# Optimization experiments

Hardware: AMD Instinct MI355X
Metric: run time of the kernel (lower is better)

## Reference

```python
import jax, jax.numpy as jnp
import numpy as np

# ---- Cl(3,0) Cayley table; blade order [1, e1,e2,e3, e12,e13,e23, e123] ----
def _build_cayley():
    blades = [0b000, 0b001, 0b010, 0b100, 0b011, 0b101, 0b110, 0b111]
    pos = {b: i for i, b in enumerate(blades)}
    def sign(a, b):
        s, a = 0, a >> 1
        while a:
            s += bin(a & b).count('1')
            a >>= 1
        return -1.0 if s & 1 else 1.0
    C = np.zeros((8, 8, 8), np.float32)
    for i, a in enumerate(blades):
        for k, b in enumerate(blades):
            C[i, pos[a ^ b], k] = sign(a, b)  # e_a * e_b -> sign * e_(a^b), metric all +1
    return jnp.asarray(C)

CAYLEY = _build_cayley()
EPS = 1e-6
SEQ = 25      # num_nodes (5) + num_edges (20)
HEADS = 8

def _expand_grades(w):
    # [..., 4] (per-grade) -> [..., 8] (per-blade), grade dims 1,3,3,1
    return jnp.concatenate([w[..., 0:1],
                            jnp.repeat(w[..., 1:2], 3, -1),
                            jnp.repeat(w[..., 2:3], 3, -1),
                            w[..., 3:4]], axis=-1)

def mv_linear(x, w, b):
    # x [N, in, 8], w [out, in, 4], b [out]; bias only on scalar blade
    y = jnp.einsum('nmi,omi->noi', x, _expand_grades(w))
    return y.at[..., 0].add(b)

def mv_layernorm(x, a):
    n = jnp.linalg.norm(x, axis=-1, keepdims=True)   # [N, c, 1] multivector norm
    n = jnp.mean(n, axis=1, keepdims=True) + EPS     # mean over channels -> [N, 1, 1]
    return a[None, :, None] * x / n

def mv_silu(x, a, b):
    # invariants: scalar component + squared grade magnitudes (mag2)
    inv = jnp.stack([x[..., 0],
                     jnp.sum(x[..., 1:4] ** 2, -1),
                     jnp.sum(x[..., 4:7] ** 2, -1),
                     x[..., 7] ** 2], axis=-1)       # [N, c, 4]
    return _expand_grades(jax.nn.sigmoid(a * inv + b)) * x

def geometric_product(a, b):
    return jnp.einsum('nci,ijk,nck->ncj', a, CAYLEY, b)


def setup_inputs() -> dict:
    key = jax.random.key(0)
    ks = iter(jax.random.split(key, 40))
    D, B = 128, 1024
    N = B * SEQ
    s = 0.05
    rn = lambda *sh: jax.random.normal(next(ks), sh, jnp.float32) * s
    return dict(
        src=jax.random.normal(next(ks), (N, D, 8), jnp.float32),
        ln1_a=jnp.ones(D, jnp.float32), ln2_a=jnp.ones(D, jnp.float32), ln3_a=jnp.ones(D, jnp.float32),
        wq=rn(D, D, 4), bq=jnp.zeros(D, jnp.float32),
        wk=rn(D, D, 4), bk=jnp.zeros(D, jnp.float32),
        wv=rn(D, D, 4), bv=jnp.zeros(D, jnp.float32),
        wo=rn(D, D, 4), bo=jnp.zeros(D, jnp.float32),
        gw1=rn(2 * D, D, 4), gb1=jnp.zeros(2 * D, jnp.float32),
        gw2=rn(2 * D, D, 4), gb2=jnp.zeros(2 * D, jnp.float32),
        gw3=rn(D, 2 * D, 4), gb3=jnp.zeros(D, jnp.float32),
        gna=jnp.ones(D, jnp.float32),
        mw1=rn(2 * D, D, 4), mb1=jnp.zeros(2 * D, jnp.float32),
        sa=jnp.ones((2 * D, 4), jnp.float32), sb=jnp.zeros((2 * D, 4), jnp.float32),
        mw2=rn(D, 2 * D, 4), mb2=jnp.zeros(D, jnp.float32),
    )


def reference(src, ln1_a, ln2_a, ln3_a, wq, bq, wk, bk, wv, bv, wo, bo,
              gw1, gb1, gw2, gb2, gw3, gb3, gna,
              mw1, mb1, sa, sb, mw2, mb2):
    N, D, _ = src.shape
    B, dh = N // SEQ, D // HEADS

    def attention(x):
        q = mv_linear(x, wq, bq).reshape(B, SEQ, HEADS, dh, 8)
        k = mv_linear(x, wk, bk).reshape(B, SEQ, HEADS, dh, 8)
        v = mv_linear(x, wv, bv).reshape(B, SEQ, HEADS, dh, 8)
        scores = jnp.einsum('bshdi,bthdi->bhst', q, k) / np.float32(np.sqrt(dh * 8))
        p = jax.nn.softmax(scores, axis=-1)
        o = jnp.einsum('bhst,bthdi->bshdi', p, v).reshape(N, D, 8)
        return mv_linear(o, wo, bo)

    # pre-norm attention + residual
    x = src + attention(mv_layernorm(src, ln1_a))
    x = mv_layernorm(x, ln2_a)
    # GP_Layer: two grade-wise linears -> geometric product -> linear -> norm
    xl = mv_linear(x, gw1, gb1)
    xr = mv_linear(x, gw2, gb2)
    g = mv_layernorm(mv_linear(geometric_product(xl, xr), gw3, gb3), gna)
    x = x + g
    x = mv_layernorm(x, ln3_a)
    # gated MLP: MVLinear -> MVSiLU -> MVLinear
    ff = mv_linear(mv_silu(mv_linear(x, mw1, mb1), sa, sb), mw2, mb2)
    return x + ff
```

## Files before the change

kernel.cpp:

```cpp
#include <hip/hip_runtime.h>
#include <hip/hip_bf16.h>
#include <math.h>

#define NROWS 25600
#define SEQL  25
#define EPSV  1e-6f

typedef __hip_bfloat16 bf16;
typedef __attribute__((ext_vector_type(4))) float f32x4;
typedef __attribute__((ext_vector_type(8))) short bf16x8;
typedef __attribute__((ext_vector_type(4))) short s16x4;
typedef unsigned int u32;

#define GLD16(gp_, lp_) __builtin_amdgcn_global_load_lds( \
    (const __attribute__((address_space(1))) u32*)(gp_), \
    (__attribute__((address_space(3))) u32*)(lp_), 16, 0, 0)

__device__ __forceinline__ float b2f(short s) {
  return __uint_as_float(((u32)(unsigned short)s) << 16);
}
__device__ __forceinline__ short f2b(float f) {
  __hip_bfloat16 h = __float2bfloat16(f);
  return *reinterpret_cast<short*>(&h);
}

__device__ __forceinline__ void gprod(const float* a, const float* b, float* r) {
  const int M[8] = {0,1,2,4,3,5,6,7};
  const int P[8] = {0,1,2,4,3,5,6,7};
#pragma unroll
  for (int i = 0; i < 8; ++i) {
    const int ma = M[i];
#pragma unroll
    for (int k = 0; k < 8; ++k) {
      const int mb = M[k];
      int par = 0;
      for (int t = ma >> 1; t; t >>= 1) par += __popc(t & mb);
      const float s = (par & 1) ? -1.f : 1.f;
      r[P[ma ^ mb]] += s * a[i] * b[k];
    }
  }
}

struct G8 {
  const bf16* A; const bf16* W; const float* bias; const float* invnm;
  bf16* Y0; bf16* Y1; bf16* Y2; bf16* Y3;
  int yc0, yc1, yc2, yc3; int ONW; int ONS;
};

#define OPITCH 84

template<int KT>
__global__ __launch_bounds__(256, 5) void gemm10_kernel(G8 P)
{
  __shared__ __align__(16) short As[64 * 128];
  __shared__ __align__(16) short Bs[64 * 128];
  const int tid  = threadIdx.x;
  const int lane = tid & 63;
  const int wid  = tid >> 6;
  const int z    = blockIdx.z;
  const int g    = (z == 0) ? 0 : ((z < 4) ? 1 : ((z < 7) ? 2 : 3));
  const int by   = blockIdx.y;
  const size_t n0 = (size_t)blockIdx.x * 64;
  const bf16* Ab = P.A + (size_t)z * NROWS * KT + n0 * KT;
  const bf16* Wb = P.W + ((size_t)g * P.ONW + by * 64) * KT;
  const int bufi = by >> 1;
  bf16* Yb; int yc;
  if      (bufi == 0) { Yb = P.Y0; yc = P.yc0; }
  else if (bufi == 1) { Yb = P.Y1; yc = P.yc1; }
  else if (bufi == 2) { Yb = P.Y2; yc = P.yc2; }
  else                { Yb = P.Y3; yc = P.yc3; }
  yc += (by & 1) * 64;

  f32x4 acc[2][2];
#pragma unroll
  for (int i = 0; i < 2; ++i)
#pragma unroll
    for (int j = 0; j < 2; ++j) acc[i][j] = (f32x4){0.f, 0.f, 0.f, 0.f};

  const int wm = (wid & 1) * 32;
  const int wn = (wid >> 1) * 32;
  const int lg  = lane >> 4;
  const int c8  = lane & 15;
  const int l15 = lane & 15;

  constexpr int NC = KT / 128;
#pragma unroll
  for (int kc = 0; kc < NC; ++kc) {
#pragma unroll
    for (int j = 0; j < 4; ++j) {
      const int row = wid * 16 + j * 4 + lg;
      const int sw = (c8 ^ (row & 7)) * 8;
      GLD16(Ab + (size_t)row * KT + kc * 128 + sw, &As[wid * 2048 + j * 512]);
      GLD16(Wb + (size_t)row * KT + kc * 128 + sw, &Bs[wid * 2048 + j * 512]);
    }
    __syncthreads();
#pragma unroll
    for (int ks = 0; ks < 4; ++ks) {
      bf16x8 af[2], bg[2];
#pragma unroll
      for (int i = 0; i < 2; ++i) {
        const int rA = wm + i * 16 + l15;
        const int rB = wn + i * 16 + l15;
        af[i] = *(const bf16x8*)&As[rA * 128 + (((ks * 4 + lg) ^ (rA & 7)) * 8)];
        bg[i] = *(const bf16x8*)&Bs[rB * 128 + (((ks * 4 + lg) ^ (rB & 7)) * 8)];
      }
#pragma unroll
      for (int mi = 0; mi < 2; ++mi)
#pragma unroll
        for (int ni = 0; ni < 2; ++ni)
          acc[mi][ni] = __builtin_amdgcn_mfma_f32_16x16x32_bf16(af[mi], bg[ni], acc[mi][ni], 0, 0, 0);
    }
    __syncthreads();
  }

  short* Os = As;
  const int cr = lg * 4;
#pragma unroll
  for (int mi = 0; mi < 2; ++mi) {
#pragma unroll
    for (int j = 0; j < 4; ++j) {
      const int r = wm + mi * 16 + cr + j;
      const size_t n = n0 + r;
      const float sc = P.invnm ? P.invnm[n] : 1.f;
#pragma unroll
      for (int ni = 0; ni < 2; ++ni) {
        const int cl = wn + ni * 16 + l15;
        float v = acc[mi][ni][j] * sc;
        if (z == 0) v += P.bias[by * 64 + cl];
        Os[r * OPITCH + cl] = f2b(v);
      }
    }
  }
  __syncthreads();

  bf16* Yp = Yb + (size_t)z * NROWS * P.ONS + yc;
  const int wrow = tid >> 3;
  const int wcol = (tid & 7) * 8;
#pragma unroll
  for (int rr = 0; rr < 2; ++rr) {
    const int row = rr * 32 + wrow;
    const s16x4 lo = *(const s16x4*)&Os[row * OPITCH + wcol];
    const s16x4 hi = *(const s16x4*)&Os[row * OPITCH + wcol + 4];
    *(s16x4*)(Yp + (size_t)(n0 + row) * P.ONS + wcol) = lo;
    *(s16x4*)(Yp + (size_t)(n0 + row) * P.ONS + wcol + 4) = hi;
  }
}

__global__ __launch_bounds__(256) void wprep_all_kernel(
    const float* wq, const float* wk, const float* wv, const float* wo,
    const float* gw1, const float* gw2, const float* gw3,
    const float* mw1, const float* mw2,
    const float* ln1, const float* ln2, const float* ln3,
    bf16* WQKV, bf16* WO, bf16* WG12, bf16* WG3, bf16* WM1, bf16* WM2)
{
  const int gid = blockIdx.x * 256 + threadIdx.x;
  const float* w; const float* ln; bf16* out; int K; int idx; int planeSz; int rowOfs;
  if      (gid <  16384) { w=wq;  ln=ln1;     out=WQKV; K=128; idx=gid;        planeSz=49152; rowOfs=0;   }
  else if (gid <  32768) { w=wk;  ln=ln1;     out=WQKV; K=128; idx=gid-16384;  planeSz=49152; rowOfs=128; }
  else if (gid <  49152) { w=wv;  ln=ln1;     out=WQKV; K=128; idx=gid-32768;  planeSz=49152; rowOfs=256; }
  else if (gid <  65536) { w=wo;  ln=nullptr; out=WO;   K=128; idx=gid-49152;  planeSz=16384; rowOfs=0;   }
  else if (gid <  98304) { w=gw1; ln=ln2;     out=WG12; K=128; idx=gid-65536;  planeSz=65536; rowOfs=0;   }
  else if (gid < 131072) { w=gw2; ln=ln2;     out=WG12; K=128; idx=gid-98304;  planeSz=65536; rowOfs=256; }
  else if (gid < 163840) { w=gw3; ln=nullptr; out=WG3;  K=256; idx=gid-131072; planeSz=32768; rowOfs=0;   }
  else if (gid < 196608) { w=mw1; ln=ln3;     out=WM1;  K=128; idx=gid-163840; planeSz=32768; rowOfs=0;   }
  else                   { w=mw2; ln=nullptr; out=WM2;  K=256; idx=gid-196608; planeSz=32768; rowOfs=0;   }
  const int k = idx % K;
  const float s = ln ? ln[k] : 1.f;
  const float4 wv4 = *(const float4*)(w + (size_t)idx * 4);
  bf16* dst = out + (size_t)rowOfs * K + idx;
  dst[0 * planeSz] = __float2bfloat16(wv4.x * s);
  dst[1 * planeSz] = __float2bfloat16(wv4.y * s);
  dst[2 * planeSz] = __float2bfloat16(wv4.z * s);
  dst[3 * planeSz] = __float2bfloat16(wv4.w * s);
}

__global__ __launch_bounds__(256) void bias_prep_kernel(
    const float* bq, const float* bk, const float* bv,
    const float* gb1, const float* gb2,
    float* BQKV, float* BG12)
{
  const int t = blockIdx.x * 256 + threadIdx.x;
  if      (t < 128) BQKV[t] = bq[t];
  else if (t < 256) BQKV[t] = bk[t - 128];
  else if (t < 384) BQKV[t] = bv[t - 256];
  else if (t < 640) BG12[t - 384] = gb1[t - 384];
  else if (t < 896) BG12[t - 384] = gb2[t - 640];
}

__global__ __launch_bounds__(256) void repack_kernel(
    const float* __restrict__ src, bf16* __restrict__ Xp, float* __restrict__ nminv)
{
  const int tid = threadIdx.x;
  const size_t base = ((size_t)blockIdx.x * 256 + tid) * 4;
  const size_t P = (size_t)NROWS * 128;
  float v[4][8];
  const float4* sp = (const float4*)(src + base * 8);
  float part = 0.f;
#pragma unroll
  for (int e = 0; e < 4; ++e) {
    const float4 a = sp[e * 2], b = sp[e * 2 + 1];
    v[e][0]=a.x; v[e][1]=a.y; v[e][2]=a.z; v[e][3]=a.w;
    v[e][4]=b.x; v[e][5]=b.y; v[e][6]=b.z; v[e][7]=b.w;
    float ss = 0.f;
#pragma unroll
    for (int p = 0; p < 8; ++p) ss += v[e][p] * v[e][p];
    part += sqrtf(ss);
  }
#pragma unroll
  for (int p = 0; p < 8; ++p) {
    s16x4 o;
#pragma unroll
    for (int e = 0; e < 4; ++e) o[e] = f2b(v[e][p]);
    *(s16x4*)(Xp + p * P + base) = o;
  }
#pragma unroll
  for (int off = 1; off < 32; off <<= 1) part += __shfl_xor(part, off);
  if ((tid & 31) == 0) nminv[base >> 7] = 1.f / (part / 128.f + EPSV);
}

__global__ __launch_bounds__(256) void attn_kernel(
    bf16* __restrict__ Q, const bf16* __restrict__ K, const bf16* __restrict__ V)
{
  __shared__ float Pld[4][32 * 36];
  const int tid  = threadIdx.x;
  const int lane = tid & 63;
  const int wid  = tid >> 6;
  const int job  = blockIdx.x * 4 + wid;
  const int b    = job >> 3;
  const int h    = job & 7;
  const size_t PS = (size_t)NROWS * 128;
  const int rowbase = b * SEQL;
  const int l15 = lane & 15;
  const int lg  = lane >> 4;

  f32x4 acc[2][2];
#pragma unroll
  for (int si = 0; si < 2; ++si)
#pragma unroll
    for (int ti = 0; ti < 2; ++ti) acc[si][ti] = (f32x4){0.f,0.f,0.f,0.f};

#pragma unroll
  for (int ks = 0; ks < 4; ++ks) {
    const int f = ks * 32 + lg * 8;
    const int p = f >> 4, d = f & 15;
    bf16x8 aq[2], bk[2];
#pragma unroll
    for (int si = 0; si < 2; ++si) {
      int s = si * 16 + l15; if (s > 24) s = 24;
      aq[si] = *(const bf16x8*)(Q + (size_t)p * PS + (size_t)(rowbase + s) * 128 + h * 16 + d);
    }
#pragma unroll
    for (int ti = 0; ti < 2; ++ti) {
      int t = ti * 16 + l15; if (t > 24) t = 24;
      bk[ti] = *(const bf16x8*)(K + (size_t)p * PS + (size_t)(rowbase + t) * 128 + h * 16 + d);
    }
#pragma unroll
    for (int si = 0; si < 2; ++si)
#pragma unroll
      for (int ti = 0; ti < 2; ++ti)
        acc[si][ti] = __builtin_amdgcn_mfma_f32_16x16x32_bf16(aq[si], bk[ti], acc[si][ti], 0, 0, 0);
  }

  const float scale = 0.08838834764831845f;
  float pv[2][2][4];
#pragma unroll
  for (int si = 0; si < 2; ++si)
#pragma unroll
    for (int ti = 0; ti < 2; ++ti)
#pragma unroll
      for (int r = 0; r < 4; ++r) {
        float v = acc[si][ti][r] * scale;
        if (ti * 16 + l15 > 24) v = -1e30f;
        pv[si][ti][r] = v;
      }
#pragma unroll
  for (int si = 0; si < 2; ++si)
#pragma unroll
    for (int r = 0; r < 4; ++r) {
      float m = fmaxf(pv[si][0][r], pv[si][1][r]);
#pragma unroll
      for (int off = 1; off < 16; off <<= 1) m = fmaxf(m, __shfl_xor(m, off));
      const float e0 = __expf(pv[si][0][r] - m);
      const float e1 = __expf(pv[si][1][r] - m);
      float sum = e0 + e1;
#pragma unroll
      for (int off = 1; off < 16; off <<= 1) sum += __shfl_xor(sum, off);
      const float inv = 1.f / sum;
      pv[si][0][r] = e0 * inv;
      pv[si][1][r] = e1 * inv;
    }

  float* Pw = &Pld[wid][0];
#pragma unroll
  for (int si = 0; si < 2; ++si)
#pragma unroll
    for (int ti = 0; ti < 2; ++ti)
#pragma unroll
      for (int r = 0; r < 4; ++r)
        Pw[(si * 16 + lg * 4 + r) * 36 + ti * 16 + l15] = pv[si][ti][r];
  __syncthreads();

  const int p2 = lane >> 3;
  const int d2 = (lane & 7) * 2;
  const bf16* vb = V + (size_t)p2 * PS + (size_t)rowbase * 128 + h * 16 + d2;
  float vlo[32], vhi[32];
#pragma unroll
  for (int t = 0; t < SEQL; ++t) {
    const __hip_bfloat162 vv = *(const __hip_bfloat162*)(vb + (size_t)t * 128);
    vlo[t] = __bfloat162float(vv.x);
    vhi[t] = __bfloat162float(vv.y);
  }
#pragma unroll
  for (int t = SEQL; t < 32; ++t) { vlo[t] = 0.f; vhi[t] = 0.f; }

  bf16* ob = Q + (size_t)p2 * PS + (size_t)rowbase * 128 + h * 16 + d2;
  for (int s = 0; s < SEQL; ++s) {
    const float4* pr = reinterpret_cast<const float4*>(&Pld[wid][s * 36]);
    float a0 = 0.f, a1 = 0.f;
#pragma unroll
    for (int t4 = 0; t4 < 8; ++t4) {
      const float4 pq = pr[t4];
      a0 += pq.x * vlo[t4*4+0] + pq.y * vlo[t4*4+1] + pq.z * vlo[t4*4+2] + pq.w * vlo[t4*4+3];
      a1 += pq.x * vhi[t4*4+0] + pq.y * vhi[t4*4+1] + pq.z * vhi[t4*4+2] + pq.w * vhi[t4*4+3];
    }
    __hip_bfloat162 o2;
    o2.x = __float2bfloat16(a0);
    o2.y = __float2bfloat16(a1);
    *(__hip_bfloat162*)(ob + (size_t)s * 128) = o2;
  }
}

__global__ __launch_bounds__(256) void xres_kernel(
    const float* __restrict__ src, const bf16* __restrict__ AO,
    bf16* __restrict__ X, float* __restrict__ nminv)
{
  const int tid = threadIdx.x;
  const size_t base = ((size_t)blockIdx.x * 256 + tid) * 4;
  const size_t P = (size_t)NROWS * 128;
  float v[4][8];
  const float4* sp = (const float4*)(src + base * 8);
#pragma unroll
  for (int e = 0; e < 4; ++e) {
    const float4 a = sp[e * 2], b = sp[e * 2 + 1];
    v[e][0]=a.x; v[e][1]=a.y; v[e][2]=a.z; v[e][3]=a.w;
    v[e][4]=b.x; v[e][5]=b.y; v[e][6]=b.z; v[e][7]=b.w;
  }
  float part = 0.f;
  float ss[4] = {0.f, 0.f, 0.f, 0.f};
#pragma unroll
  for (int p = 0; p < 8; ++p) {
    const s16x4 av = *(const s16x4*)(AO + p * P + base);
    s16x4 o;
#pragma unroll
    for (int e = 0; e < 4; ++e) {
      v[e][p] += b2f(av[e]);
      o[e] = f2b(v[e][p]);
      ss[e] += v[e][p] * v[e][p];
    }
    *(s16x4*)(X + p * P + base) = o;
  }
#pragma unroll
  for (int e = 0; e < 4; ++e) part += sqrtf(ss[e]);
#pragma unroll
  for (int off = 1; off < 32; off <<= 1) part += __shfl_xor(part, off);
  if ((tid & 31) == 0) nminv[base >> 7] = 1.f / (part / 128.f + EPSV);
}

__global__ __launch_bounds__(256) void gp_kernel(
    bf16* __restrict__ XL, const bf16* __restrict__ XR)
{
  const size_t base = ((size_t)blockIdx.x * 256 + threadIdx.x) * 4;
  const size_t P = (size_t)NROWS * 256;
  s16x4 av[8], bv[8], rv[8];
#pragma unroll
  for (int p = 0; p < 8; ++p) {
    av[p] = *(const s16x4*)(XL + p * P + base);
    bv[p] = *(const s16x4*)(XR + p * P + base);
  }
#pragma unroll
  for (int e = 0; e < 4; ++e) {
    float a[8], b[8], r[8] = {0.f,0.f,0.f,0.f,0.f,0.f,0.f,0.f};
#pragma unroll
    for (int p = 0; p < 8; ++p) { a[p] = b2f(av[p][e]); b[p] = b2f(bv[p][e]); }
    gprod(a, b, r);
#pragma unroll
    for (int p = 0; p < 8; ++p) rv[p][e] = f2b(r[p]);
  }
#pragma unroll
  for (int p = 0; p < 8; ++p) *(s16x4*)(XL + p * P + base) = rv[p];
}

__global__ __launch_bounds__(256) void combine_kernel(
    bf16* __restrict__ X, const bf16* __restrict__ Gl,
    const float* __restrict__ ln2a, const float* __restrict__ gna,
    const float* __restrict__ nm2inv, float* __restrict__ nm4inv)
{
  const int tid = threadIdx.x;
  const size_t base = ((size_t)blockIdx.x * 256 + tid) * 4;
  const size_t P = (size_t)NROWS * 128;
  const size_t n = base >> 7;
  const int c = (int)(base & 127);

  float gv[4][8];
  float ssg[4] = {0.f,0.f,0.f,0.f};
#pragma unroll
  for (int p = 0; p < 8; ++p) {
    const s16x4 g4 = *(const s16x4*)(Gl + p * P + base);
#pragma unroll
    for (int e = 0; e < 4; ++e) { gv[e][p] = b2f(g4[e]); ssg[e] += gv[e][p] * gv[e][p]; }
  }
  float partg = sqrtf(ssg[0]) + sqrtf(ssg[1]) + sqrtf(ssg[2]) + sqrtf(ssg[3]);
#pragma unroll
  for (int off = 1; off < 32; off <<= 1) partg += __shfl_xor(partg, off);
  const float invg = 1.f / (partg / 128.f + EPSV);

  const float n2 = nm2inv[n];
  float s2[4], sg[4];
#pragma unroll
  for (int e = 0; e < 4; ++e) { s2[e] = ln2a[c + e] * n2; sg[e] = gna[c + e] * invg; }

  float ss[4] = {0.f,0.f,0.f,0.f};
#pragma unroll
  for (int p = 0; p < 8; ++p) {
    const s16x4 x4 = *(const s16x4*)(X + p * P + base);
    s16x4 o;
#pragma unroll
    for (int e = 0; e < 4; ++e) {
      const float v = s2[e] * b2f(x4[e]) + sg[e] * gv[e][p];
      o[e] = f2b(v);
      ss[e] += v * v;
    }
    *(s16x4*)(X + p * P + base) = o;
  }
  float part = sqrtf(ss[0]) + sqrtf(ss[1]) + sqrtf(ss[2]) + sqrtf(ss[3]);
#pragma unroll
  for (int off = 1; off < 32; off <<= 1) part += __shfl_xor(part, off);
  if ((tid & 31) == 0) nm4inv[n] = 1.f / (part / 128.f + EPSV);
}

__global__ __launch_bounds__(256) void silu_kernel(
    bf16* __restrict__ H, const float* __restrict__ sa, const float* __restrict__ sb)
{
  const size_t base = ((size_t)blockIdx.x * 256 + threadIdx.x) * 4;
  const int c = (int)(base & 255);
  const size_t P = (size_t)NROWS * 256;
  s16x4 hv[8];
#pragma unroll
  for (int p = 0; p < 8; ++p) hv[p] = *(const s16x4*)(H + p * P + base);
#pragma unroll
  for (int e = 0; e < 4; ++e) {
    float v[8];
#pragma unroll
    for (int p = 0; p < 8; ++p) v[p] = b2f(hv[p][e]);
    const float i0 = v[0];
    const float i1 = v[1]*v[1] + v[2]*v[2] + v[3]*v[3];
    const float i2 = v[4]*v[4] + v[5]*v[5] + v[6]*v[6];
    const float i3 = v[7]*v[7];
    const int cc = c + e;
    const float g0 = 1.f / (1.f + __expf(-(sa[cc*4+0]*i0 + sb[cc*4+0])));
    const float g1 = 1.f / (1.f + __expf(-(sa[cc*4+1]*i1 + sb[cc*4+1])));
    const float g2 = 1.f / (1.f + __expf(-(sa[cc*4+2]*i2 + sb[cc*4+2])));
    const float g3 = 1.f / (1.f + __expf(-(sa[cc*4+3]*i3 + sb[cc*4+3])));
    v[0]*=g0; v[1]*=g1; v[2]*=g1; v[3]*=g1; v[4]*=g2; v[5]*=g2; v[6]*=g2; v[7]*=g3;
#pragma unroll
    for (int p = 0; p < 8; ++p) hv[p][e] = f2b(v[p]);
  }
#pragma unroll
  for (int p = 0; p < 8; ++p) *(s16x4*)(H + p * P + base) = hv[p];
}

__global__ __launch_bounds__(256) void final_kernel(
    const bf16* __restrict__ X3, const bf16* __restrict__ FF,
    const float* __restrict__ ln3a, const float* __restrict__ nm4inv,
    float* __restrict__ out)
{
  const size_t base = ((size_t)blockIdx.x * 256 + threadIdx.x) * 4;
  const int c = (int)(base & 127);
  const size_t n = base >> 7;
  const size_t P = (size_t)NROWS * 128;
  const float nm = nm4inv[n];
  float o[4][8];
#pragma unroll
  for (int p = 0; p < 8; ++p) {
    const s16x4 x4 = *(const s16x4*)(X3 + p * P + base);
    const s16x4 f4 = *(const s16x4*)(FF + p * P + base);
#pragma unroll
    for (int e = 0; e < 4; ++e)
      o[e][p] = ln3a[c + e] * nm * b2f(x4[e]) + b2f(f4[e]);
  }
  float4* op = (float4*)(out + base * 8);
#pragma unroll
  for (int e = 0; e < 4; ++e) {
    float4 lo, hi;
    lo.x=o[e][0]; lo.y=o[e][1]; lo.z=o[e][2]; lo.w=o[e][3];
    hi.x=o[e][4]; hi.y=o[e][5]; hi.z=o[e][6]; hi.w=o[e][7];
    op[e * 2] = lo;
    op[e * 2 + 1] = hi;
  }
}

extern "C" void kernel_launch(void* const* d_in, const int* in_sizes, int n_in,
                              void* d_out, int out_size, void* d_ws, size_t ws_size,
                              hipStream_t stream) {
  (void)in_sizes; (void)n_in; (void)out_size; (void)ws_size;
  const float* src   = (const float*)d_in[0];
  const float* ln1_a = (const float*)d_in[1];
  const float* ln2_a = (const float*)d_in[2];
  const float* ln3_a = (const float*)d_in[3];
  const float* wq = (const float*)d_in[4];  const float* bq = (const float*)d_in[5];
  const float* wk = (const float*)d_in[6];  const float* bk = (const float*)d_in[7];
  const float* wv = (const float*)d_in[8];  const float* bv = (const float*)d_in[9];
  const float* wo = (const float*)d_in[10]; const float* bo = (const float*)d_in[11];
  const float* gw1 = (const float*)d_in[12]; const float* gb1 = (const float*)d_in[13];
  const float* gw2 = (const float*)d_in[14]; const float* gb2 = (const float*)d_in[15];
  const float* gw3 = (const float*)d_in[16]; const float* gb3 = (const float*)d_in[17];
  const float* gna = (const float*)d_in[18];
  const float* mw1 = (const float*)d_in[19]; const float* mb1 = (const float*)d_in[20];
  const float* sa  = (const float*)d_in[21]; const float* sb  = (const float*)d_in[22];
  const float* mw2 = (const float*)d_in[23]; const float* mb2 = (const float*)d_in[24];

  char* ws = (char*)d_ws;
  const size_t P128 = (size_t)NROWS * 128;
  const size_t PSET = 8 * P128;
  bf16* R1 = (bf16*)ws;
  bf16* R2 = (bf16*)(ws + 104857600);
  bf16* WQKV = (bf16*)(ws + 157286400);
  bf16* WO   = WQKV + 196608;
  bf16* WG12 = WO   + 65536;
  bf16* WG3  = WG12 + 262144;
  bf16* WM1  = WG3  + 131072;
  bf16* WM2  = WM1  + 131072;
  float* BQKV = (float*)(ws + 159121408);
  float* BG12 = BQKV + 384;
  float* nm1  = BG12 + 512;
  float* nm2  = nm1 + NROWS;
  float* nm4  = nm2 + NROWS;

  bf16* Dd = (bf16*)d_out;
  bf16* Kb = R1;
  bf16* Vb = R1 + PSET;

  wprep_all_kernel<<<896, 256, 0, stream>>>(
      wq, wk, wv, wo, gw1, gw2, gw3, mw1, mw2, ln1_a, ln2_a, ln3_a,
      WQKV, WO, WG12, WG3, WM1, WM2);
  bias_prep_kernel<<<4, 256, 0, stream>>>(bq, bk, bv, gb1, gb2, BQKV, BG12);

  repack_kernel<<<3200, 256, 0, stream>>>(src, R2, nm1);

  G8 P{};
  P = G8{R2, WQKV, BQKV, nm1, Dd, Kb, Vb, nullptr, 0,0,0,0, 384, 128};
  gemm10_kernel<128><<<dim3(400, 6, 8), 256, 0, stream>>>(P);

  attn_kernel<<<2048, 256, 0, stream>>>(Dd, Kb, Vb);

  P = G8{Dd, WO, bo, nullptr, R1, nullptr, nullptr, nullptr, 0,0,0,0, 128, 128};
  gemm10_kernel<128><<<dim3(400, 2, 8), 256, 0, stream>>>(P);

  xres_kernel<<<3200, 256, 0, stream>>>(src, R1, R2, nm2);

  P = G8{R2, WG12, BG12, nm2, Dd, Dd, R1, R1, 0, 128, 0, 128, 512, 256};
  gemm10_kernel<128><<<dim3(400, 8, 8), 256, 0, stream>>>(P);

  gp_kernel<<<6400, 256, 0, stream>>>(Dd, R1);

  P = G8{Dd, WG3, gb3, nullptr, R1, nullptr, nullptr, nullptr, 0,0,0,0, 128, 128};
  gemm10_kernel<256><<<dim3(400, 2, 8), 256, 0, stream>>>(P);

  combine_kernel<<<3200, 256, 0, stream>>>(R2, R1, ln2_a, gna, nm2, nm4);

  P = G8{R2, WM1, mb1, nm4, Dd, Dd, nullptr, nullptr, 0, 128, 0, 0, 256, 256};
  gemm10_kernel<128><<<dim3(400, 4, 8), 256, 0, stream>>>(P);

  silu_kernel<<<6400, 256, 0, stream>>>(Dd, sa, sb);

  P = G8{Dd, WM2, mb2, nullptr, R1, nullptr, nullptr, nullptr, 0,0,0,0, 128, 128};
  gemm10_kernel<256><<<dim3(400, 2, 8), 256, 0, stream>>>(P);

  final_kernel<<<3200, 256, 0, stream>>>(R2, R1, ln3_a, nm4, (float*)d_out);
}
```

Before: 583.0 us.

## Keep A tile resident in LDS and loop over output column tiles in-block

The GEMM kernel now stages the 64-row activation tile once into shared memory and loops over all output column tiles inside the block, restaging only the weight tile per column tile. Previously each column tile was a separate block that reloaded the same activation rows. This cuts the number of blocks and the redundant global reads of activations. In exchange, shared memory per block grows (up to 64 KB+ for KT=256), occupancy drops (launch bounds hint removed), and the weight restage is not overlapped with compute.

```diff
diff --git a/kernel.cpp b/kernel.cpp
--- a/kernel.cpp
+++ b/kernel.cpp
@@ -41,7 +41,7 @@
   }
 }
 
-struct G8 {
+struct G11 {
   const bf16* A; const bf16* W; const float* bias; const float* invnm;
   bf16* Y0; bf16* Y1; bf16* Y2; bf16* Y3;
   int yc0, yc1, yc2, yc3; int ONW; int ONS;
@@ -49,100 +49,115 @@
 
 #define OPITCH 84
 
-template<int KT>
-__global__ __launch_bounds__(256, 5) void gemm10_kernel(G8 P)
-{
-  __shared__ __align__(16) short As[64 * 128];
-  __shared__ __align__(16) short Bs[64 * 128];
+template<int KT, int NCOL>
+__global__ __launch_bounds__(256) void gemm11_kernel(G11 P)
+{
+  constexpr int NC = KT / 128;
+  __shared__ __align__(16) short As[64 * KT];
+  __shared__ __align__(16) short Ws[64 * KT];
+  __shared__ __align__(16) short Cs[64 * OPITCH];
   const int tid  = threadIdx.x;
   const int lane = tid & 63;
   const int wid  = tid >> 6;
   const int z    = blockIdx.z;
   const int g    = (z == 0) ? 0 : ((z < 4) ? 1 : ((z < 7) ? 2 : 3));
-  const int by   = blockIdx.y;
   const size_t n0 = (size_t)blockIdx.x * 64;
   const bf16* Ab = P.A + (size_t)z * NROWS * KT + n0 * KT;
-  const bf16* Wb = P.W + ((size_t)g * P.ONW + by * 64) * KT;
-  const int bufi = by >> 1;
-  bf16* Yb; int yc;
-  if      (bufi == 0) { Yb = P.Y0; yc = P.yc0; }
-  else if (bufi == 1) { Yb = P.Y1; yc = P.yc1; }
-  else if (bufi == 2) { Yb = P.Y2; yc = P.yc2; }
-  else                { Yb = P.Y3; yc = P.yc3; }
-  yc += (by & 1) * 64;
-
-  f32x4 acc[2][2];
-#pragma unroll
-  for (int i = 0; i < 2; ++i)
-#pragma unroll
-    for (int j = 0; j < 2; ++j) acc[i][j] = (f32x4){0.f, 0.f, 0.f, 0.f};
-
-  const int wm = (wid & 1) * 32;
-  const int wn = (wid >> 1) * 32;
+  const int wm  = (wid & 1) * 32;
+  const int wn  = (wid >> 1) * 32;
   const int lg  = lane >> 4;
-  const int c8  = lane & 15;
   const int l15 = lane & 15;
 
-  constexpr int NC = KT / 128;
-#pragma unroll
-  for (int kc = 0; kc < NC; ++kc) {
+  auto STAGEW = [&](int ct) {
+    const bf16* Wb = P.W + ((size_t)g * P.ONW + ct * 64) * KT;
+#pragma unroll
+    for (int kc = 0; kc < NC; ++kc)
+#pragma unroll
+      for (int j = 0; j < 4; ++j) {
+        const int row = wid * 16 + j * 4 + lg;
+        const int sw = (l15 ^ (row & 7)) * 8;
+        GLD16(Wb + (size_t)row * KT + kc * 128 + sw, &Ws[kc * 8192 + wid * 2048 + j * 512]);
+      }
+  };
+
+#pragma unroll
+  for (int kc = 0; kc < NC; ++kc)
 #pragma unroll
     for (int j = 0; j < 4; ++j) {
       const int row = wid * 16 + j * 4 + lg;
-      const int sw = (c8 ^ (row & 7)) * 8;
-      GLD16(Ab + (size_t)row * KT + kc * 128 + sw, &As[wid * 2048 + j * 512]);
-      GLD16(Wb + (size_t)row * KT + kc * 128 + sw, &Bs[wid * 2048 + j * 512]);
+      const int sw = (l15 ^ (row & 7)) * 8;
+      GLD16(Ab + (size_t)row * KT + kc * 128 + sw, &As[kc * 8192 + wid * 2048 + j * 512]);
+    }
+  STAGEW(0);
+  __syncthreads();
+
+#pragma unroll
+  for (int ct = 0; ct < NCOL; ++ct) {
+    f32x4 acc[2][2];
+#pragma unroll
+    for (int i = 0; i < 2; ++i)
+#pragma unroll
+      for (int j = 0; j < 2; ++j) acc[i][j] = (f32x4){0.f, 0.f, 0.f, 0.f};
+#pragma unroll
+    for (int kc = 0; kc < NC; ++kc) {
+#pragma unroll
+      for (int ks = 0; ks < 4; ++ks) {
+        bf16x8 af[2], bg[2];
+#pragma unroll
+        for (int i = 0; i < 2; ++i) {
+          const int rA = wm + i * 16 + l15;
+          const int rB = wn + i * 16 + l15;
+          af[i] = *(const bf16x8*)&As[kc * 8192 + rA * 128 + (((ks * 4 + lg) ^ (rA & 7)) * 8)];
+          bg[i] = *(const bf16x8*)&Ws[kc * 8192 + rB * 128 + (((ks * 4 + lg) ^ (rB & 7)) * 8)];
+        }
+#pragma unroll
+        for (int mi = 0; mi < 2; ++mi)
+#pragma unroll
+          for (int ni = 0; ni < 2; ++ni)
+            acc[mi][ni] = __builtin_amdgcn_mfma_f32_16x16x32_bf16(af[mi], bg[ni], acc[mi][ni], 0, 0, 0);
+      }
+    }
+
+    const int cr = lg * 4;
+#pragma unroll
+    for (int mi = 0; mi < 2; ++mi) {
+#pragma unroll
+      for (int j = 0; j < 4; ++j) {
+        const int r = wm + mi * 16 + cr + j;
+        const size_t n = n0 + r;
+        const float sc = P.invnm ? P.invnm[n] : 1.f;
+#pragma unroll
+        for (int ni = 0; ni < 2; ++ni) {
+          const int cl = wn + ni * 16 + l15;
+          float v = acc[mi][ni][j] * sc;
+          if (z == 0) v += P.bias[ct * 64 + cl];
+          Cs[r * OPITCH + cl] = f2b(v);
+        }
+      }
     }
     __syncthreads();
-#pragma unroll
-    for (int ks = 0; ks < 4; ++ks) {
-      bf16x8 af[2], bg[2];
-#pragma unroll
-      for (int i = 0; i < 2; ++i) {
-        const int rA = wm + i * 16 + l15;
-        const int rB = wn + i * 16 + l15;
-        af[i] = *(const bf16x8*)&As[rA * 128 + (((ks * 4 + lg) ^ (rA & 7)) * 8)];
-        bg[i] = *(const bf16x8*)&Bs[rB * 128 + (((ks * 4 + lg) ^ (rB & 7)) * 8)];
-      }
-#pragma unroll
-      for (int mi = 0; mi < 2; ++mi)
-#pragma unroll
-        for (int ni = 0; ni < 2; ++ni)
-          acc[mi][ni] = __builtin_amdgcn_mfma_f32_16x16x32_bf16(af[mi], bg[ni], acc[mi][ni], 0, 0, 0);
+
+    if (ct + 1 < NCOL) STAGEW(ct + 1);
+
+    const int bufi = ct >> 1;
+    bf16* Yb; int yc;
+    if      (bufi == 0) { Yb = P.Y0; yc = P.yc0; }
+    else if (bufi == 1) { Yb = P.Y1; yc = P.yc1; }
+    else if (bufi == 2) { Yb = P.Y2; yc = P.yc2; }
+    else                { Yb = P.Y3; yc = P.yc3; }
+    yc += (ct & 1) * 64;
+    bf16* Yp = Yb + (size_t)z * NROWS * P.ONS + yc;
+    const int wrow = tid >> 3;
+    const int wcol = (tid & 7) * 8;
+#pragma unroll
+    for (int rr = 0; rr < 2; ++rr) {
+      const int row = rr * 32 + wrow;
+      const s16x4 lo = *(const s16x4*)&Cs[row * OPITCH + wcol];
+      const s16x4 hi = *(const s16x4*)&Cs[row * OPITCH + wcol + 4];
+      *(s16x4*)(Yp + (size_t)(n0 + row) * P.ONS + wcol) = lo;
+      *(s16x4*)(Yp + (size_t)(n0 + row) * P.ONS + wcol + 4) = hi;
     }
     __syncthreads();
-  }
-
-  short* Os = As;
-  const int cr = lg * 4;
-#pragma unroll
-  for (int mi = 0; mi < 2; ++mi) {
-#pragma unroll
-    for (int j = 0; j < 4; ++j) {
-      const int r = wm + mi * 16 + cr + j;
-      const size_t n = n0 + r;
-      const float sc = P.invnm ? P.invnm[n] : 1.f;
-#pragma unroll
-      for (int ni = 0; ni < 2; ++ni) {
-        const int cl = wn + ni * 16 + l15;
-        float v = acc[mi][ni][j] * sc;
-        if (z == 0) v += P.bias[by * 64 + cl];
-        Os[r * OPITCH + cl] = f2b(v);
-      }
-    }
-  }
-  __syncthreads();
-
-  bf16* Yp = Yb + (size_t)z * NROWS * P.ONS + yc;
-  const int wrow = tid >> 3;
-  const int wcol = (tid & 7) * 8;
-#pragma unroll
-  for (int rr = 0; rr < 2; ++rr) {
-    const int row = rr * 32 + wrow;
-    const s16x4 lo = *(const s16x4*)&Os[row * OPITCH + wcol];
-    const s16x4 hi = *(const s16x4*)&Os[row * OPITCH + wcol + 4];
-    *(s16x4*)(Yp + (size_t)(n0 + row) * P.ONS + wcol) = lo;
-    *(s16x4*)(Yp + (size_t)(n0 + row) * P.ONS + wcol + 4) = hi;
   }
 }
 
@@ -547,34 +562,34 @@
 
   repack_kernel<<<3200, 256, 0, stream>>>(src, R2, nm1);
 
-  G8 P{};
-  P = G8{R2, WQKV, BQKV, nm1, Dd, Kb, Vb, nullptr, 0,0,0,0, 384, 128};
-  gemm10_kernel<128><<<dim3(400, 6, 8), 256, 0, stream>>>(P);
+  G11 P{};
+  P = G11{R2, WQKV, BQKV, nm1, Dd, Kb, Vb, nullptr, 0,0,0,0, 384, 128};
+  gemm11_kernel<128, 6><<<dim3(400, 1, 8), 256, 0, stream>>>(P);
 
   attn_kernel<<<2048, 256, 0, stream>>>(Dd, Kb, Vb);
 
-  P = G8{Dd, WO, bo, nullptr, R1, nullptr, nullptr, nullptr, 0,0,0,0, 128, 128};
-  gemm10_kernel<128><<<dim3(400, 2, 8), 256, 0, stream>>>(P);
+  P = G11{Dd, WO, bo, nullptr, R1, nullptr, nullptr, nullptr, 0,0,0,0, 128, 128};
+  gemm11_kernel<128, 2><<<dim3(400, 1, 8), 256, 0, stream>>>(P);
 
   xres_kernel<<<3200, 256, 0, stream>>>(src, R1, R2, nm2);
 
-  P = G8{R2, WG12, BG12, nm2, Dd, Dd, R1, R1, 0, 128, 0, 128, 512, 256};
-  gemm10_kernel<128><<<dim3(400, 8, 8), 256, 0, stream>>>(P);
+  P = G11{R2, WG12, BG12, nm2, Dd, Dd, R1, R1, 0, 128, 0, 128, 512, 256};
+  gemm11_kernel<128, 8><<<dim3(400, 1, 8), 256, 0, stream>>>(P);
 
   gp_kernel<<<6400, 256, 0, stream>>>(Dd, R1);
 
-  P = G8{Dd, WG3, gb3, nullptr, R1, nullptr, nullptr, nullptr, 0,0,0,0, 128, 128};
-  gemm10_kernel<256><<<dim3(400, 2, 8), 256, 0, stream>>>(P);
+  P = G11{Dd, WG3, gb3, nullptr, R1, nullptr, nullptr, nullptr, 0,0,0,0, 128, 128};
+  gemm11_kernel<256, 2><<<dim3(400, 1, 8), 256, 0, stream>>>(P);
 
   combine_kernel<<<3200, 256, 0, stream>>>(R2, R1, ln2_a, gna, nm2, nm4);
 
-  P = G8{R2, WM1, mb1, nm4, Dd, Dd, nullptr, nullptr, 0, 128, 0, 0, 256, 256};
-  gemm10_kernel<128><<<dim3(400, 4, 8), 256, 0, stream>>>(P);
+  P = G11{R2, WM1, mb1, nm4, Dd, Dd, nullptr, nullptr, 0, 128, 0, 0, 256, 256};
+  gemm11_kernel<128, 4><<<dim3(400, 1, 8), 256, 0, stream>>>(P);
 
   silu_kernel<<<6400, 256, 0, stream>>>(Dd, sa, sb);
 
-  P = G8{Dd, WM2, mb2, nullptr, R1, nullptr, nullptr, nullptr, 0,0,0,0, 128, 128};
-  gemm10_kernel<256><<<dim3(400, 2, 8), 256, 0, stream>>>(P);
+  P = G11{Dd, WM2, mb2, nullptr, R1, nullptr, nullptr, nullptr, 0,0,0,0, 128, 128};
+  gemm11_kernel<256, 2><<<dim3(400, 1, 8), 256, 0, stream>>>(P);
 
   final_kernel<<<3200, 256, 0, stream>>>(R2, R1, ln3_a, nm4, (float*)d_out);
 }
```

After: 603.1 us. +3.4%, slower.
